# Kernel optimization log

Hardware: AMD Instinct MI355X
Metric: run time of the kernel (lower is better)

## Reference

```python
import jax, jax.numpy as jnp
import numpy as np

B, N, NC = 16, 25200, 80          # batch, raw predictions, classes (COCO)
CONF_THRES = 0.25
IOU_THRES = 0.45
MAX_CAND = 1000                    # candidates kept after score top-k (pre-NMS)
CLS_OFFSET = 4096.0                # class-wise box offset (non-agnostic NMS trick)
EPS = 1e-7


def setup_inputs() -> dict:
    key = jax.random.key(0)
    # raw head output: [x, y, w, h, obj, cls0..cls79], values in [0,1]
    pred = jax.random.uniform(key, (B, N, 5 + NC), dtype=jnp.float32)
    return {"pred": pred}


def _xywh2xyxy(x):
    xy, wh = x[..., :2], x[..., 2:4]
    return jnp.concatenate([xy - wh * 0.5, xy + wh * 0.5], axis=-1)


def _box_iou(boxes):
    # boxes: [C, 4] xyxy -> pairwise IoU [C, C]
    area = (boxes[:, 2] - boxes[:, 0]) * (boxes[:, 3] - boxes[:, 1])
    lt = jnp.maximum(boxes[:, None, :2], boxes[None, :, :2])
    rb = jnp.minimum(boxes[:, None, 2:], boxes[None, :, 2:])
    wh = jnp.clip(rb - lt, 0.0)
    inter = wh[..., 0] * wh[..., 1]
    return inter / (area[:, None] + area[None, :] - inter + EPS)


def _nms_single(p):
    # p: [N, 5+NC] -> (out [MAX_CAND, 6] xyxy/conf/cls zero-padded, keep [MAX_CAND] bool)
    obj = p[:, 4]
    cls_scores = p[:, 5:] * obj[:, None]          # conf = obj * cls
    conf = jnp.max(cls_scores, axis=-1)
    cls_idx = jnp.argmax(cls_scores, axis=-1)
    valid = (obj > CONF_THRES) & (conf > CONF_THRES)
    score = jnp.where(valid, conf, -1.0)

    # pre-NMS top-k by score (sorted descending) — fixed-shape stand-in for boolean filter
    top_scores, idx = jax.lax.top_k(score, MAX_CAND)
    boxes = _xywh2xyxy(p[idx, :4])                # [C, 4]
    kconf = conf[idx]
    kcls = cls_idx[idx].astype(jnp.float32)
    valid_c = top_scores > 0.0

    # class-offset boxes so different classes never overlap (agnostic=False)
    off_boxes = boxes + kcls[:, None] * CLS_OFFSET
    iou = _box_iou(off_boxes)                     # [C, C]

    ar = jnp.arange(MAX_CAND)

    def body(i, keep):
        sup = keep[i] & (iou[i] > IOU_THRES) & (ar > i)
        return keep & jnp.logical_not(sup)

    keep = jax.lax.fori_loop(0, MAX_CAND, body, valid_c)

    out = jnp.concatenate([boxes, kconf[:, None], kcls[:, None]], axis=-1)  # [C, 6]
    out = jnp.where(keep[:, None], out, 0.0)
    return out, keep


def reference(pred):
    out, keep = jax.vmap(_nms_single)(pred)
    return out, keep
```

## Files before the change

kernel.cpp:

```cpp
#include <hip/hip_runtime.h>
#include <stdint.h>

typedef unsigned int u32;
typedef unsigned long long u64;

#define BATCH 16
#define NANCH 25200
#define NCLS 80
#define ROWF 85
#define MAXC 1000
#define CONF_T 0.25f
#define IOU_T 0.45f
#define EPS_F 1e-7f
#define TILE 64
#define NTILES ((NANCH + TILE - 1) / TILE)

__device__ __forceinline__ float iou_ref(float4 a, float4 b) {
#pragma clang fp contract(off)
  float ai = (a.z - a.x) * (a.w - a.y);
  float aj = (b.z - b.x) * (b.w - b.y);
  float ltx = fmaxf(a.x, b.x), lty = fmaxf(a.y, b.y);
  float rbx = fminf(a.z, b.z), rby = fminf(a.w, b.w);
  float wx = fmaxf(rbx - ltx, 0.0f), wy = fmaxf(rby - lty, 0.0f);
  float inter = wx * wy;
  return inter / (ai + aj - inter + EPS_F);
}

__global__ __launch_bounds__(256) void k1_score(const float* __restrict__ pred,
                                                u32* __restrict__ keys32) {
  __shared__ float srow[TILE * ROWF];
  __shared__ u32 skeys[TILE];
  int tid = threadIdx.x;
  int b = blockIdx.y;
  int t0 = blockIdx.x * TILE;
  int ntile = (t0 + TILE <= NANCH) ? TILE : (NANCH - t0);
  int nf4 = (ntile * ROWF) >> 2;

  const float4* src4 = (const float4*)(pred + ((size_t)b * NANCH + t0) * ROWF);
  float4* smem4 = (float4*)srow;
#pragma unroll
  for (int k = 0; k < 6; ++k) {
    int i = k * 256 + tid;
    if (i < nf4) smem4[i] = src4[i];
  }
  __syncthreads();

  int a = tid >> 2;
  int q = tid & 3;
  float best = -1e30f;
  int bidx = 0;
  float obj = 0.0f;
  if (a < ntile) {
    const float* row = srow + a * ROWF;
    obj = row[4];
    int c0 = q * 20;
#pragma unroll
    for (int c = 0; c < 20; ++c) {
      float s = row[5 + c0 + c] * obj;
      if (s > best) { best = s; bidx = c0 + c; }
    }
  }
#pragma unroll
  for (int off = 1; off < 4; off <<= 1) {
    float ob = __shfl_xor(best, off);
    int oi = __shfl_xor(bidx, off);
    if (ob > best || (ob == best && oi < bidx)) { best = ob; bidx = oi; }
  }
  if (q == 0 && a < ntile) {
    bool valid = (obj > CONF_T) && (best > CONF_T);
    u32 k = valid ? (((__float_as_uint(best) - 0x3E800000u) << 7) | (u32)bidx)
                  : 0u;
    skeys[a] = k;
  }
  __syncthreads();
  if (tid < ntile) keys32[(size_t)b * NANCH + t0 + tid] = skeys[tid];
}

__global__ __launch_bounds__(1024) void k2_select(const float* __restrict__ pred,
                                                  const u32* __restrict__ keys32,
                                                  float* __restrict__ selbox,
                                                  float* __restrict__ offbox,
                                                  float2* __restrict__ selmeta) {
  int b = blockIdx.x;
  int tid = threadIdx.x;
  int wv = tid >> 6, lane = tid & 63;
  __shared__ u32 h[8192];
  __shared__ u64 skey[2048];
  __shared__ u32 wsum[16];
  __shared__ u32 sh_fbin;
  __shared__ u32 scount;

  const u32* kb = keys32 + (size_t)b * NANCH;
  u32 kreg[25];
#pragma unroll
  for (int j = 0; j < 25; ++j) {
    int i = tid + j * 1024;
    kreg[j] = (i < NANCH) ? kb[i] : 0u;
  }
  for (int i = tid; i < 8192; i += 1024) h[i] = 0;
  if (tid == 0) { sh_fbin = 0; scount = 0; }
  skey[tid] = ~0ull;
  skey[tid + 1024] = ~0ull;
  __syncthreads();
#pragma unroll
  for (int j = 0; j < 25; ++j) {
    u32 k = kreg[j];
    if (k >= 0x80u) atomicAdd(&h[k >> 18], 1u);
  }
  __syncthreads();
  u32 a[8]; u32 lsum = 0;
#pragma unroll
  for (int k = 0; k < 8; ++k) { a[k] = h[8 * tid + k]; lsum += a[k]; }
  u32 suf = lsum;
#pragma unroll
  for (int off = 1; off < 64; off <<= 1) {
    u32 tv = __shfl_down(suf, off);
    if (lane + off < 64) suf += tv;
  }
  if (lane == 0) wsum[wv] = suf;
  __syncthreads();
  u32 base = 0;
#pragma unroll
  for (int w2 = 0; w2 < 16; ++w2) if (w2 > wv) base += wsum[w2];
  u32 e = base + suf - lsum;
#pragma unroll
  for (int k = 7; k >= 0; --k) {
    u32 inc = e + a[k];
    if ((int)inc >= MAXC && (int)e < MAXC) sh_fbin = (u32)(8 * tid + k);
    e = inc;
  }
  __syncthreads();
  u32 cut = sh_fbin << 18;
#pragma unroll
  for (int j = 0; j < 25; ++j) {
    u32 k = kreg[j];
    if (k >= cut && k != 0u) {
      int i = tid + j * 1024;
      u64 sk = ((u64)(k >> 7) << 32) |
               (u64)(((32767u - (u32)i) << 7) | (k & 127u));
      u32 p = atomicAdd(&scount, 1u);
      if (p < 2048) skey[p] = ~sk;
    }
  }
  __syncthreads();
  int n = (scount <= 1024u) ? 1024 : 2048;
  for (u32 kk = 2; kk <= (u32)n; kk <<= 1) {
    for (u32 j = kk >> 1; j > 0; j >>= 1) {
      for (int idx = tid; idx < n; idx += 1024) {
        u32 ixj = (u32)idx ^ j;
        if (ixj > (u32)idx) {
          u64 x = skey[idx], y = skey[ixj];
          bool up = ((idx & kk) == 0);
          if (up ? (x > y) : (x < y)) { skey[idx] = y; skey[ixj] = x; }
        }
      }
      __syncthreads();
    }
  }
  if (tid < MAXC) {
    u64 k = ~skey[tid];
    u32 confpart = (u32)(k >> 32);
    u32 lo = (u32)k;
    bool valid = confpart != 0u;
    float conf = 0.0f, x1 = 0.0f, y1 = 0.0f, x2 = 0.0f, y2 = 0.0f;
    float cf = 0.0f, offv = 0.0f;
    if (valid) {
      u32 nidx = 32767u - ((lo >> 7) & 0x7FFFu);
      u32 ci = lo & 127u;
      conf = __uint_as_float(confpart + 0x3E800000u);
      const float* pr = pred + ((size_t)b * NANCH + nidx) * ROWF;
      float x = pr[0], y = pr[1], w = pr[2], h2 = pr[3];
      x1 = x - w * 0.5f; y1 = y - h2 * 0.5f;
      x2 = x + w * 0.5f; y2 = y + h2 * 0.5f;
      cf = (float)ci; offv = cf * 4096.0f;
    }
    int o = b * MAXC + tid;
    ((float4*)selbox)[o] = make_float4(x1, y1, x2, y2);
    ((float4*)offbox)[o] = make_float4(x1 + offv, y1 + offv, x2 + offv, y2 + offv);
    selmeta[o] = make_float2(conf, cf);
  }
}

__global__ __launch_bounds__(256) void k3_dt(const float4* __restrict__ offbox4,
                                             u64* __restrict__ dt) {
  int wid = blockIdx.x * 4 + (threadIdx.x >> 6);
  int lane = threadIdx.x & 63;
  int b = wid / MAXC;
  int i = wid % MAXC;
  float4 bi = offbox4[b * MAXC + i];
  u64 myword = 0;
  for (int w = 0; w < 16; ++w) {
    int j = w * 64 + lane;
    int jc = (j < MAXC) ? j : 0;
    float4 bj = offbox4[b * MAXC + jc];
    float iou = iou_ref(bi, bj);
    bool bit = (iou > IOU_T) && (j < i);
    u64 bal = __ballot(bit ? 1 : 0);
    if (lane == w) myword = bal;
  }
  if (lane < 16) dt[((size_t)b * 16 + lane) * MAXC + i] = myword;
}

__global__ __launch_bounds__(1024) void k4_jacobi(const u64* __restrict__ dt,
                                                  const float2* __restrict__ selmeta,
                                                  const float* __restrict__ selbox,
                                                  float* __restrict__ out) {
  int b = blockIdx.x;
  int tid = threadIdx.x;
  int wv = tid >> 6, lane = tid & 63;
  __shared__ u64 keepv[16];
  __shared__ u32 changed;
  bool valid = false;
  float2 meta = make_float2(0.0f, 0.0f);
  u64 dtr[16];
  if (tid < MAXC) {
    meta = selmeta[b * MAXC + tid];
    valid = meta.x > 0.0f;
#pragma unroll
    for (int w = 0; w < 16; ++w) dtr[w] = dt[((size_t)b * 16 + w) * MAXC + tid];
  } else {
#pragma unroll
    for (int w = 0; w < 16; ++w) dtr[w] = 0ull;
  }
  u64 bal0 = __ballot(valid ? 1 : 0);
  if (tid == 0) changed = 0;
  if (lane == 0) keepv[wv] = bal0;
  __syncthreads();
  for (int pass = 0; pass < MAXC; ++pass) {
    u64 kv[16];
#pragma unroll
    for (int w = 0; w < 16; ++w) kv[w] = keepv[w];
    u64 s = 0;
#pragma unroll
    for (int w = 0; w < 16; ++w) s |= dtr[w] & kv[w];
    bool nk = valid && (s == 0ull);
    u64 bal = __ballot(nk ? 1 : 0);
    __syncthreads();
    if (lane == 0 && bal != kv[wv]) { keepv[wv] = bal; atomicOr(&changed, 1u); }
    __syncthreads();
    u32 ch = changed;
    __syncthreads();
    if (tid == 0) changed = 0;
    if (!ch) break;
  }
  if (tid < MAXC) {
    bool kept = ((keepv[wv] >> lane) & 1ull) != 0ull;
    size_t o = (size_t)b * MAXC + tid;
    float4 bx = ((const float4*)selbox)[o];
    float* orow = out + o * 6;
    orow[0] = kept ? bx.x : 0.0f;
    orow[1] = kept ? bx.y : 0.0f;
    orow[2] = kept ? bx.z : 0.0f;
    orow[3] = kept ? bx.w : 0.0f;
    orow[4] = kept ? meta.x : 0.0f;
    orow[5] = kept ? meta.y : 0.0f;
    out[(size_t)BATCH * MAXC * 6 + o] = kept ? 1.0f : 0.0f;
  }
}

extern "C" void kernel_launch(void* const* d_in, const int* in_sizes, int n_in,
                              void* d_out, int out_size, void* d_ws, size_t ws_size,
                              hipStream_t stream) {
  const float* pred = (const float*)d_in[0];
  float* out = (float*)d_out;
  char* ws = (char*)d_ws;
  size_t off = 0;
  auto alloc = [&](size_t bytes) -> void* {
    void* p = ws + off;
    off = (off + bytes + 255) & ~(size_t)255;
    return p;
  };
  u32* keys32   = (u32*)alloc((size_t)BATCH * NANCH * 4);
  float* selbox = (float*)alloc((size_t)BATCH * MAXC * 4 * 4);
  float* offbox = (float*)alloc((size_t)BATCH * MAXC * 4 * 4);
  float2* selmeta = (float2*)alloc((size_t)BATCH * MAXC * 8);
  u64* dt       = (u64*)alloc((size_t)BATCH * 16 * MAXC * 8);
  (void)ws_size; (void)in_sizes; (void)n_in; (void)out_size;

  dim3 g1(NTILES, BATCH);
  k1_score<<<g1, 256, 0, stream>>>(pred, keys32);
  k2_select<<<BATCH, 1024, 0, stream>>>(pred, keys32, selbox, offbox, selmeta);
  k3_dt<<<(BATCH * MAXC) / 4, 256, 0, stream>>>((const float4*)offbox, dt);
  k4_jacobi<<<BATCH, 1024, 0, stream>>>(dt, selmeta, selbox, out);
}
```

Baseline: 244.5 us.

## Use register/shuffle bitonic sort and double-buffer Jacobi change flag

For the common case of at most 1024 candidates, the bitonic sort keeps each key in a register. It uses wavefront shuffles for strides below 64 and goes through shared memory only for larger strides, which cuts block-wide barriers and LDS traffic. The Jacobi NMS loop now double-buffers its convergence flag, which removes one __syncthreads per pass. The 2048-key fallback path is left as it was. The shuffle path adds two barriers per large-stride step, and correctness depends on the ping-pong flag being reset before it is reused.

```diff
diff --git a/kernel.cpp b/kernel.cpp
--- a/kernel.cpp
+++ b/kernel.cpp
@@ -143,22 +143,45 @@
     }
   }
   __syncthreads();
-  int n = (scount <= 1024u) ? 1024 : 2048;
-  for (u32 kk = 2; kk <= (u32)n; kk <<= 1) {
-    for (u32 j = kk >> 1; j > 0; j >>= 1) {
-      for (int idx = tid; idx < n; idx += 1024) {
-        u32 ixj = (u32)idx ^ j;
-        if (ixj > (u32)idx) {
-          u64 x = skey[idx], y = skey[ixj];
-          bool up = ((idx & kk) == 0);
-          if (up ? (x > y) : (x < y)) { skey[idx] = y; skey[ixj] = x; }
+  u64 v;
+  if (scount <= 1024u) {
+    v = skey[tid];
+    for (u32 kk = 2; kk <= 1024; kk <<= 1) {
+      for (u32 j = kk >> 1; j > 0; j >>= 1) {
+        bool up = ((tid & kk) == 0);
+        bool low = ((tid & j) == 0);
+        if (j >= 64) {
+          skey[tid] = v;
+          __syncthreads();
+          u64 o = skey[tid ^ j];
+          bool takemin = (up == low);
+          v = takemin ? (v < o ? v : o) : (v > o ? v : o);
+          __syncthreads();
+        } else {
+          u64 o = __shfl_xor(v, (int)j);
+          bool takemin = (up == low);
+          v = takemin ? (v < o ? v : o) : (v > o ? v : o);
         }
       }
-      __syncthreads();
-    }
+    }
+  } else {
+    for (u32 kk = 2; kk <= 2048; kk <<= 1) {
+      for (u32 j = kk >> 1; j > 0; j >>= 1) {
+        for (int idx = tid; idx < 2048; idx += 1024) {
+          u32 ixj = (u32)idx ^ j;
+          if (ixj > (u32)idx) {
+            u64 x = skey[idx], y = skey[ixj];
+            bool up = ((idx & kk) == 0);
+            if (up ? (x > y) : (x < y)) { skey[idx] = y; skey[ixj] = x; }
+          }
+        }
+        __syncthreads();
+      }
+    }
+    v = skey[tid];
   }
   if (tid < MAXC) {
-    u64 k = ~skey[tid];
+    u64 k = ~v;
     u32 confpart = (u32)(k >> 32);
     u32 lo = (u32)k;
     bool valid = confpart != 0u;
@@ -209,7 +232,7 @@
   int tid = threadIdx.x;
   int wv = tid >> 6, lane = tid & 63;
   __shared__ u64 keepv[16];
-  __shared__ u32 changed;
+  __shared__ u32 changed2[2];
   bool valid = false;
   float2 meta = make_float2(0.0f, 0.0f);
   u64 dtr[16];
@@ -223,7 +246,7 @@
     for (int w = 0; w < 16; ++w) dtr[w] = 0ull;
   }
   u64 bal0 = __ballot(valid ? 1 : 0);
-  if (tid == 0) changed = 0;
+  if (tid == 0) { changed2[0] = 0; changed2[1] = 0; }
   if (lane == 0) keepv[wv] = bal0;
   __syncthreads();
   for (int pass = 0; pass < MAXC; ++pass) {
@@ -236,11 +259,13 @@
     bool nk = valid && (s == 0ull);
     u64 bal = __ballot(nk ? 1 : 0);
     __syncthreads();
-    if (lane == 0 && bal != kv[wv]) { keepv[wv] = bal; atomicOr(&changed, 1u); }
+    if (lane == 0 && bal != kv[wv]) {
+      keepv[wv] = bal;
+      atomicOr(&changed2[pass & 1], 1u);
+    }
     __syncthreads();
-    u32 ch = changed;
-    __syncthreads();
-    if (tid == 0) changed = 0;
+    u32 ch = changed2[pass & 1];
+    if (tid == 0) changed2[(pass & 1) ^ 1] = 0;
     if (!ch) break;
   }
   if (tid < MAXC) {
```

Result: no change. 241.4 us (-1.3%).
